# Kernel tuning notes

Measured on AMD Instinct MI355X. Metric: run time of the kernel, lower is better.

The kernel has to match this reference:

```python
import jax, jax.numpy as jnp
import numpy as np

B, T, C = 32, 512, 1024
H, D = 16, 64
BLOCK_SIZE = 512


def setup_inputs() -> dict:
    key = jax.random.key(0)
    ks = jax.random.split(key, 6)
    s_in = 1.0 / np.sqrt(C)
    return {
        "x": jax.random.normal(ks[0], (B, T, C), dtype=jnp.float32),
        "wq": jax.random.normal(ks[1], (H, C, D), dtype=jnp.float32) * s_in,
        "wk": jax.random.normal(ks[2], (H, C, D), dtype=jnp.float32) * s_in,
        "wv": jax.random.normal(ks[3], (H, C, D), dtype=jnp.float32) * s_in,
        "w_proj": jax.random.normal(ks[4], (C, C), dtype=jnp.float32) * s_in,
        "b_proj": jax.random.normal(ks[5], (C,), dtype=jnp.float32) * 0.01,
    }


def reference(x, wq, wk, wv, w_proj, b_proj):
    b, t, c = x.shape
    # per-head projections (bias=False Linears stacked on head axis)
    q = jnp.einsum("btc,hcd->bhtd", x, wq)
    k = jnp.einsum("btc,hcd->bhtd", x, wk)
    v = jnp.einsum("btc,hcd->bhtd", x, wv)
    # NOTE: original scales by 1/sqrt(C) with C = n_embd, not head_size
    scale = 1.0 / (c ** 0.5)
    scores = jnp.einsum("bhtd,bhsd->bhts", q, k) * scale  # [B,H,T,T]
    causal = jnp.tril(jnp.ones((t, t), dtype=bool))
    scores = jnp.where(causal, scores, jnp.finfo(scores.dtype).min)
    attn = jax.nn.softmax(scores, axis=-1)
    out = jnp.einsum("bhts,bhsd->bhtd", attn, v)
    # concat heads in order -> [B,T,H*D]
    out = out.transpose(0, 2, 1, 3).reshape(b, t, -1)
    # output projection (dropout = identity in eval mode)
    return out @ w_proj + b_proj
```

## Files before the change

### kernel.cpp

```cpp
#include <hip/hip_runtime.h>

typedef unsigned int u32;
typedef unsigned short u16;
typedef __bf16 bf16x8 __attribute__((ext_vector_type(8)));
typedef float f32x4 __attribute__((ext_vector_type(4)));
typedef u16 u16x8 __attribute__((ext_vector_type(8)));
typedef u16 u16x4 __attribute__((ext_vector_type(4)));

#define DEVI static __device__ __forceinline__

DEVI u16 f2bf(float f) {
  union { float f; u32 u; } v; v.f = f;
  return (u16)((v.u + 0x7fffu + ((v.u >> 16) & 1u)) >> 16);
}

DEVI u32 cvtpk(float a, float b) {
  u32 r;
  asm("v_cvt_pk_bf16_f32 %0, %1, %2" : "=v"(r) : "v"(a), "v"(b));
  return r;
}

constexpr long QS_ = 16777216;
constexpr long XB_O    = 0;
constexpr long WQKV_O  = 16777216;
constexpr long Q_O     = 19922944;
constexpr long CTX_O   = 70254592;
constexpr long WPROJ_O = 87031808;

__global__ __launch_bounds__(256) void k_prep_all(const float* __restrict__ x,
                                                  const float* __restrict__ wq,
                                                  const float* __restrict__ wk,
                                                  const float* __restrict__ wv,
                                                  const float* __restrict__ wp,
                                                  u16* __restrict__ ws) {
  __shared__ float tile[64][65];
  const int b = blockIdx.x;
  const int tid = threadIdx.x;
  if (b < 1024) {
    const float* src;
    u16* dst;
    long srs;
    if (b < 768) {
      int sel = b >> 8, rest = b & 255, h = rest >> 4, kt = rest & 15;
      const float* W = (sel == 0) ? wq : ((sel == 1) ? wk : wv);
      src = W + (long)(h * 1024 + kt * 64) * 64;
      srs = 64;
      dst = ws + WQKV_O + (long)(sel * 1024 + h * 64) * 1024 + kt * 64;
    } else {
      int b3 = b - 768, ntile = b3 >> 4, kt = b3 & 15;
      src = wp + (long)(kt * 64) * 1024 + ntile * 64;
      srs = 1024;
      dst = ws + WPROJ_O + (long)(ntile * 64) * 1024 + kt * 64;
    }
    #pragma unroll
    for (int i = 0; i < 4; ++i) {
      int idx = i * 256 + tid, r = idx >> 4, c4 = idx & 15;
      float4 v = *(const float4*)(src + (long)r * srs + c4 * 4);
      tile[r][c4 * 4 + 0] = v.x; tile[r][c4 * 4 + 1] = v.y;
      tile[r][c4 * 4 + 2] = v.z; tile[r][c4 * 4 + 3] = v.w;
    }
    __syncthreads();
    #pragma unroll
    for (int i = 0; i < 2; ++i) {
      int idx = i * 256 + tid, dr = idx >> 3, c8 = idx & 7;
      u16x8 o8;
      #pragma unroll
      for (int j = 0; j < 8; ++j) o8[j] = f2bf(tile[c8 * 8 + j][dr]);
      *(u16x8*)(dst + (long)dr * 1024 + c8 * 8) = o8;
    }
  } else {
    long id = (long)(b - 1024) * 256 + tid;
    const float4* p = (const float4*)(x + id * 8);
    float4 a = p[0], c = p[1];
    u16x8 r;
    r[0]=f2bf(a.x); r[1]=f2bf(a.y); r[2]=f2bf(a.z); r[3]=f2bf(a.w);
    r[4]=f2bf(c.x); r[5]=f2bf(c.y); r[6]=f2bf(c.z); r[7]=f2bf(c.w);
    *(u16x8*)(ws + XB_O + id * 8) = r;
  }
}

DEVI void gload16(const u16* g, u16* l) {
  __builtin_amdgcn_global_load_lds((const __attribute__((address_space(1))) u32*)g,
                                   (__attribute__((address_space(3))) u32*)l, 16, 0, 0);
}

template <int NN, int EPI>
__global__ __launch_bounds__(512, 2)
void k_gemm(const u16* __restrict__ A, const u16* __restrict__ Bt,
            u16* __restrict__ oq, float* __restrict__ of, const float* __restrict__ bias) {
  __shared__ u16 lds[2][4][8192];

  const int tid = threadIdx.x;
  const int lane = tid & 63;
  const int w = tid >> 6;
  const int wm = w >> 2, wn = w & 3;
  const int lg = lane >> 4, lr = lane & 15;
  const int bht = 2 + (wn >> 1);
  const int bn0 = (wn & 1) * 4;

  constexpr int NBN = NN / 256;
  const int nwg = gridDim.x;
  const int swz = ((int)blockIdx.x & 7) * (nwg >> 3) + ((int)blockIdx.x >> 3);
  const long m0 = (long)(swz / NBN) * 256, n0 = (long)(swz % NBN) * 256;

  int srcoff[2];
  #pragma unroll
  for (int r2 = 0; r2 < 2; ++r2) {
    int s = r2 * 8 + w;
    int mi = s >> 1, ks = s & 1;
    int rowl = mi * 16 + (lane >> 2);
    int colu = ks * 32 + (((lane & 3) * 8) ^ (((lane >> 5) & 1) * 16));
    srcoff[r2] = rowl * 1024 + colu;
  }
  const int fo = lr * 32 + ((lg * 8) ^ (((lr >> 3) & 1) * 16));

  const u16* At  = A  + m0 * 1024;
  const u16* Bt2 = Bt + n0 * 1024;

  f32x4 acc[8][4] = {};
  bf16x8 aq[2][2][2];
  bf16x8 bfr[4][2];

#define STAGE(buf_, ht_, gbase_)                                               \
  { _Pragma("unroll") for (int r_ = 0; r_ < 2; ++r_)                           \
      gload16((gbase_) + srcoff[r_], &lds[buf_][ht_][r_ * 4096 + w * 512]); }

#define LDS_AQ(set_, buf_, q_)                                                 \
  { _Pragma("unroll") for (int i_ = 0; i_ < 2; ++i_)                           \
    _Pragma("unroll") for (int ks_ = 0; ks_ < 2; ++ks_)                        \
      aq[set_][i_][ks_] = *(const bf16x8*)&lds[buf_][wm][(((q_)*2 + i_) * 2 + ks_) * 512 + fo]; }

#define LDS_BF(buf_, lo_)                                                      \
  { _Pragma("unroll") for (int j_ = 0; j_ < 2; ++j_)                           \
    _Pragma("unroll") for (int ks_ = 0; ks_ < 2; ++ks_)                        \
      bfr[(lo_) + j_][ks_] = *(const bf16x8*)&lds[buf_][bht][((bn0 + (lo_) + j_) * 2 + ks_) * 512 + fo]; }

#define QUAD8(set_, q_, lo_)                                                   \
  { __builtin_amdgcn_s_setprio(1);                                             \
    _Pragma("unroll") for (int ks_ = 0; ks_ < 2; ++ks_)                        \
    _Pragma("unroll") for (int i_ = 0; i_ < 2; ++i_)                           \
    _Pragma("unroll") for (int j_ = 0; j_ < 2; ++j_)                           \
      acc[(q_)*2 + i_][(lo_) + j_] = __builtin_amdgcn_mfma_f32_16x16x32_bf16(  \
          aq[set_][i_][ks_], bfr[(lo_) + j_][ks_], acc[(q_)*2 + i_][(lo_) + j_], 0, 0, 0); \
    __builtin_amdgcn_s_setprio(0); }

#define BARF() { asm volatile("s_barrier" ::: "memory"); }

  STAGE(0, 0, At);
  STAGE(0, 1, At + 131072);
  STAGE(0, 2, Bt2);
  STAGE(0, 3, Bt2 + 131072);
  STAGE(1, 0, At + 64);
  STAGE(1, 1, At + 131072 + 64);
  STAGE(1, 2, Bt2 + 64);
  STAGE(1, 3, Bt2 + 131072 + 64);
  asm volatile("s_waitcnt vmcnt(8)" ::: "memory");
  BARF();
  LDS_AQ(0, 0, 0);
  LDS_BF(0, 0);

  #pragma unroll 1
  for (int t = 0; t < 16; ++t) {
    const int buf = t & 1;
    LDS_BF(buf, 2);
    LDS_AQ(1, buf, 1);
    QUAD8(0, 0, 0);
    BARF();
    QUAD8(0, 0, 2);
    BARF();
    LDS_AQ(0, buf, 2);
    if (t + 2 < 16) { STAGE(buf, 2, Bt2 + (t + 2) * 64); STAGE(buf, 3, Bt2 + 131072 + (t + 2) * 64); }
    QUAD8(1, 1, 0);
    BARF();
    QUAD8(1, 1, 2);
    BARF();
    LDS_AQ(1, buf, 3);
    QUAD8(0, 2, 0);
    BARF();
    QUAD8(0, 2, 2);
    asm volatile("s_waitcnt lgkmcnt(0)" ::: "memory");
    __builtin_amdgcn_sched_barrier(0);
    BARF();
    if (t + 2 < 16) { STAGE(buf, 0, At + (t + 2) * 64); STAGE(buf, 1, At + 131072 + (t + 2) * 64); }
    QUAD8(1, 3, 0);
    BARF();
    if (t < 14)       { asm volatile("s_waitcnt vmcnt(8)" ::: "memory"); }
    else if (t == 14) { asm volatile("s_waitcnt vmcnt(0)" ::: "memory"); }
    BARF();
    if (t + 1 < 16) {
      LDS_AQ(0, buf ^ 1, 0);
      LDS_BF(buf ^ 1, 0);
    }
    QUAD8(1, 3, 2);
    BARF();
  }

  if constexpr (EPI == 0) {
    #pragma unroll
    for (int mi = 0; mi < 8; ++mi) {
      int grow = (int)m0 + wm * 128 + mi * 16 + lg * 4;
      int b = grow >> 9, t0 = grow & 511;
      #pragma unroll
      for (int ni = 0; ni < 4; ++ni) {
        int gcol = (int)n0 + wn * 64 + ni * 16 + lr;
        int sel = gcol >> 10, h = (gcol >> 6) & 15, d = gcol & 63;
        u16* dst = oq + (long)sel * QS_ + (((long)(b * 16 + h) * 512 + t0) * 64 + d);
        #pragma unroll
        for (int r = 0; r < 4; ++r) dst[r * 64] = f2bf(acc[mi][ni][r]);
      }
    }
  } else {
    float bv[4];
    #pragma unroll
    for (int ni = 0; ni < 4; ++ni) bv[ni] = bias[(int)n0 + wn * 64 + ni * 16 + lr];
    #pragma unroll
    for (int mi = 0; mi < 8; ++mi) {
      int grow = (int)m0 + wm * 128 + mi * 16 + lg * 4;
      #pragma unroll
      for (int ni = 0; ni < 4; ++ni) {
        int gcol = (int)n0 + wn * 64 + ni * 16 + lr;
        #pragma unroll
        for (int r = 0; r < 4; ++r)
          of[(long)(grow + r) * NN + gcol] = acc[mi][ni][r] + bv[ni];
      }
    }
  }
#undef STAGE
#undef LDS_AQ
#undef LDS_BF
#undef QUAD8
#undef BARF
}

__global__ __launch_bounds__(256, 3)
void k_attn(const u16* __restrict__ Qp, const u16* __restrict__ Kp,
            const u16* __restrict__ Vp, u16* __restrict__ ctx) {
  __shared__ u16 k_lds[2][64 * 72];
  __shared__ u16 vt_lds[2][64 * 72];

  const int bid = blockIdx.x;
  const int qi = 3 - (bid >> 9);
  const int bh = bid & 511;
  const int tid = threadIdx.x, lane = tid & 63, w = tid >> 6;
  const int lg = lane >> 4, lr = lane & 15;
  const long base = (long)bh * (512 * 64);

  const int q0 = qi * 128 + w * 32;

  bf16x8 qf[2][2];
  #pragma unroll
  for (int mt = 0; mt < 2; ++mt)
    #pragma unroll
    for (int k2 = 0; k2 < 2; ++k2)
      qf[mt][k2] = *(const bf16x8*)(Qp + base + (long)(q0 + mt * 16 + lr) * 64 + k2 * 32 + lg * 8);

  f32x4 o[2][4] = {};
  float ls[2] = {0.f, 0.f};
  u32 pkw[2][4][2];

  const int nch = (qi + 1) * 2;
  int srow[2], scol[2], cslot[2];
  #pragma unroll
  for (int i = 0; i < 2; ++i) {
    int s = i * 256 + tid;
    srow[i] = s >> 3; scol[i] = s & 7;
    int sr = srow[i];
    cslot[i] = ((sr >> 5) << 5) + (((sr >> 2) & 3) << 3) + (((sr >> 4) & 1) << 2) + (sr & 3);
  }

  uint4 kreg[2], vreg[2];
  auto loadch = [&](int c) {
    #pragma unroll
    for (int i = 0; i < 2; ++i) {
      long go = base + (long)(c * 64 + srow[i]) * 64 + scol[i] * 8;
      kreg[i] = *(const uint4*)(Kp + go);
      vreg[i] = *(const uint4*)(Vp + go);
    }
  };
  auto writech = [&](int bsel) {
    #pragma unroll
    for (int i = 0; i < 2; ++i) {
      *(uint4*)&k_lds[bsel][srow[i] * 72 + scol[i] * 8] = kreg[i];
      union { uint4 v; u16 s[8]; } t; t.v = vreg[i];
      #pragma unroll
      for (int j = 0; j < 8; ++j)
        vt_lds[bsel][(scol[i] * 8 + j) * 72 + cslot[i]] = t.s[j];
    }
  };
  auto pv_step = [&](int vsel) {
    bf16x8 vf2[4][2];
    #pragma unroll
    for (int dt = 0; dt < 4; ++dt)
      #pragma unroll
      for (int k2 = 0; k2 < 2; ++k2)
        vf2[dt][k2] = *(const bf16x8*)&vt_lds[vsel][(dt * 16 + lr) * 72 + k2 * 32 + lg * 8];
    __builtin_amdgcn_s_setprio(1);
    #pragma unroll
    for (int k2 = 0; k2 < 2; ++k2)
      #pragma unroll
      for (int mt = 0; mt < 2; ++mt) {
        union { u32 w4[4]; bf16x8 v; } pb;
        pb.w4[0] = pkw[mt][2 * k2][0];
        pb.w4[1] = pkw[mt][2 * k2][1];
        pb.w4[2] = pkw[mt][2 * k2 + 1][0];
        pb.w4[3] = pkw[mt][2 * k2 + 1][1];
        #pragma unroll
        for (int dt = 0; dt < 4; ++dt)
          o[mt][dt] = __builtin_amdgcn_mfma_f32_16x16x32_bf16(vf2[dt][k2], pb.v, o[mt][dt], 0, 0, 0);
      }
    __builtin_amdgcn_s_setprio(0);
  };

  loadch(0);
  writech(0);
  loadch(1);
  __syncthreads();

  const float sc = 0.045084220027780106f;

  #pragma unroll 1
  for (int c = 0; c < nch; ++c) {
    const int bsel = c & 1;
    const bool doQK = (c * 64 <= q0 + 31);
    const bool doPV = (c >= 1) && ((c - 1) * 64 <= q0 + 31);

    f32x4 st[2][4] = {};
    if (doQK) {
      bf16x8 kf2[4][2];
      #pragma unroll
      for (int nt = 0; nt < 4; ++nt)
        #pragma unroll
        for (int k2 = 0; k2 < 2; ++k2)
          kf2[nt][k2] = *(const bf16x8*)&k_lds[bsel][(nt * 16 + lr) * 72 + k2 * 32 + lg * 8];
      __builtin_amdgcn_s_setprio(1);
      #pragma unroll
      for (int k2 = 0; k2 < 2; ++k2)
        #pragma unroll
        for (int mt = 0; mt < 2; ++mt)
          #pragma unroll
          for (int nt = 0; nt < 4; ++nt)
            st[mt][nt] = __builtin_amdgcn_mfma_f32_16x16x32_bf16(kf2[nt][k2], qf[mt][k2], st[mt][nt], 0, 0, 0);
      __builtin_amdgcn_s_setprio(0);
    }

    if (doPV) pv_step(bsel ^ 1);

    if (doQK) {
      const bool full = (c * 64 + 63 <= q0);
      #pragma unroll
      for (int mt = 0; mt < 2; ++mt) {
        const int q = q0 + mt * 16 + lr;
        if (!full) {
          #pragma unroll
          for (int nt = 0; nt < 4; ++nt)
            #pragma unroll
            for (int r = 0; r < 4; ++r) {
              int s_ = c * 64 + nt * 16 + lg * 4 + r;
              st[mt][nt][r] = (s_ <= q) ? st[mt][nt][r] : -1e30f;
            }
        }
        float ps = 0.f;
        float p[4][4];
        #pragma unroll
        for (int nt = 0; nt < 4; ++nt)
          #pragma unroll
          for (int r = 0; r < 4; ++r) {
            float pv = exp2f(st[mt][nt][r] * sc);
            p[nt][r] = pv;
            ps += pv;
          }
        ls[mt] += ps;
        #pragma unroll
        for (int nt = 0; nt < 4; ++nt) {
          pkw[mt][nt][0] = cvtpk(p[nt][0], p[nt][1]);
          pkw[mt][nt][1] = cvtpk(p[nt][2], p[nt][3]);
        }
      }
    }

    __syncthreads();
    if (c + 1 < nch) writech(bsel ^ 1);
    if (c + 2 < nch) loadch(c + 2);
    __syncthreads();
  }

  if ((nch - 1) * 64 <= q0 + 31) pv_step((nch - 1) & 1);

  const int b = bh >> 4, h = bh & 15;
  #pragma unroll
  for (int mt = 0; mt < 2; ++mt) {
    float l = ls[mt];
    l += __shfl_xor(l, 16);
    l += __shfl_xor(l, 32);
    const float inv = 1.0f / l;
    const int t = q0 + mt * 16 + lr;
    #pragma unroll
    for (int dt = 0; dt < 4; ++dt) {
      u16x4 pk4;
      #pragma unroll
      for (int r = 0; r < 4; ++r) pk4[r] = f2bf(o[mt][dt][r] * inv);
      *(u16x4*)(ctx + ((long)(b * 512 + t)) * 1024 + h * 64 + dt * 16 + lg * 4) = pk4;
    }
  }
}

extern "C" void kernel_launch(void* const* d_in, const int* in_sizes, int n_in,
                              void* d_out, int out_size, void* d_ws, size_t ws_size,
                              hipStream_t stream) {
  const float* x  = (const float*)d_in[0];
  const float* wq = (const float*)d_in[1];
  const float* wk = (const float*)d_in[2];
  const float* wv = (const float*)d_in[3];
  const float* wp = (const float*)d_in[4];
  const float* bp = (const float*)d_in[5];
  float* out = (float*)d_out;
  u16* ws = (u16*)d_ws;

  u16* XB    = ws + XB_O;
  u16* WQKV  = ws + WQKV_O;
  u16* Qb    = ws + Q_O;
  u16* CTX   = ws + CTX_O;
  u16* WPROJ = ws + WPROJ_O;

  k_prep_all<<<9216, 256, 0, stream>>>(x, wq, wk, wv, wp, ws);
  k_gemm<3072, 0><<<(16384 / 256) * (3072 / 256), 512, 0, stream>>>(XB, WQKV, Qb, nullptr, nullptr);
  k_attn<<<2048, 256, 0, stream>>>(Qb, Qb + QS_, Qb + 2 * QS_, CTX);
  k_gemm<1024, 1><<<(16384 / 256) * (1024 / 256), 512, 0, stream>>>(CTX, WPROJ, nullptr, out, bp);
}
```

Measured before the change: 221.7 us.

## Load GEMM B fragments from global memory, fold softmax scale into Q, stagger V transpose

The GEMM no longer stages the B (weight) tile through LDS. Each wave loads its B fragments directly from global memory into registers, which halves LDS usage and drops the B staging loads and their waits. The softmax scale (log2e/sqrt(C)) is now folded into the Q epilogue of the QKV GEMM, removing one multiply per score in attention. The V transpose write into LDS rotates its element order per column to reduce bank conflicts. Direct global B loads skip the LDS reuse across waves and may raise global/L2 traffic and latency exposure.

New measurement: 340.4 us. 1.54x slower.

```diff
diff --git a/kernel.cpp b/kernel.cpp
--- a/kernel.cpp
+++ b/kernel.cpp
@@ -26,6 +26,8 @@
 constexpr long Q_O     = 19922944;
 constexpr long CTX_O   = 70254592;
 constexpr long WPROJ_O = 87031808;
+
+#define SCL_Q 0.045084220027780106f
 
 __global__ __launch_bounds__(256) void k_prep_all(const float* __restrict__ x,
                                                   const float* __restrict__ wq,
@@ -88,15 +90,15 @@
 __global__ __launch_bounds__(512, 2)
 void k_gemm(const u16* __restrict__ A, const u16* __restrict__ Bt,
             u16* __restrict__ oq, float* __restrict__ of, const float* __restrict__ bias) {
-  __shared__ u16 lds[2][4][8192];
+  __shared__ u16 lds[2][2][8192];
 
   const int tid = threadIdx.x;
   const int lane = tid & 63;
   const int w = tid >> 6;
   const int wm = w >> 2, wn = w & 3;
   const int lg = lane >> 4, lr = lane & 15;
-  const int bht = 2 + (wn >> 1);
   const int bn0 = (wn & 1) * 4;
+  const int bhtrow = (wn >> 1) * 128;
 
   constexpr int NBN = NN / 256;
   const int nwg = gridDim.x;
@@ -116,6 +118,7 @@
 
   const u16* At  = A  + m0 * 1024;
   const u16* Bt2 = Bt + n0 * 1024;
+  const u16* Bfb = Bt2 + (long)(bhtrow + bn0 * 16 + lr) * 1024 + lg * 8;
 
   f32x4 acc[8][4] = {};
   bf16x8 aq[2][2][2];
@@ -130,10 +133,10 @@
     _Pragma("unroll") for (int ks_ = 0; ks_ < 2; ++ks_)                        \
       aq[set_][i_][ks_] = *(const bf16x8*)&lds[buf_][wm][(((q_)*2 + i_) * 2 + ks_) * 512 + fo]; }
 
-#define LDS_BF(buf_, lo_)                                                      \
+#define GLB_BF(t_, lo_)                                                        \
   { _Pragma("unroll") for (int j_ = 0; j_ < 2; ++j_)                           \
     _Pragma("unroll") for (int ks_ = 0; ks_ < 2; ++ks_)                        \
-      bfr[(lo_) + j_][ks_] = *(const bf16x8*)&lds[buf_][bht][((bn0 + (lo_) + j_) * 2 + ks_) * 512 + fo]; }
+      bfr[(lo_) + j_][ks_] = *(const bf16x8*)(Bfb + ((lo_) + j_) * 16384 + (t_) * 64 + ks_ * 32); }
 
 #define QUAD8(set_, q_, lo_)                                                   \
   { __builtin_amdgcn_s_setprio(1);                                             \
@@ -148,28 +151,23 @@
 
   STAGE(0, 0, At);
   STAGE(0, 1, At + 131072);
-  STAGE(0, 2, Bt2);
-  STAGE(0, 3, Bt2 + 131072);
   STAGE(1, 0, At + 64);
   STAGE(1, 1, At + 131072 + 64);
-  STAGE(1, 2, Bt2 + 64);
-  STAGE(1, 3, Bt2 + 131072 + 64);
-  asm volatile("s_waitcnt vmcnt(8)" ::: "memory");
+  asm volatile("s_waitcnt vmcnt(4)" ::: "memory");
   BARF();
+  GLB_BF(0, 0);
   LDS_AQ(0, 0, 0);
-  LDS_BF(0, 0);
 
   #pragma unroll 1
   for (int t = 0; t < 16; ++t) {
     const int buf = t & 1;
-    LDS_BF(buf, 2);
+    GLB_BF(t, 2);
     LDS_AQ(1, buf, 1);
     QUAD8(0, 0, 0);
     BARF();
     QUAD8(0, 0, 2);
     BARF();
     LDS_AQ(0, buf, 2);
-    if (t + 2 < 16) { STAGE(buf, 2, Bt2 + (t + 2) * 64); STAGE(buf, 3, Bt2 + 131072 + (t + 2) * 64); }
     QUAD8(1, 1, 0);
     BARF();
     QUAD8(1, 1, 2);
@@ -184,12 +182,12 @@
     if (t + 2 < 16) { STAGE(buf, 0, At + (t + 2) * 64); STAGE(buf, 1, At + 131072 + (t + 2) * 64); }
     QUAD8(1, 3, 0);
     BARF();
-    if (t < 14)       { asm volatile("s_waitcnt vmcnt(8)" ::: "memory"); }
+    if (t < 14)       { asm volatile("s_waitcnt vmcnt(4)" ::: "memory"); }
     else if (t == 14) { asm volatile("s_waitcnt vmcnt(0)" ::: "memory"); }
     BARF();
     if (t + 1 < 16) {
+      GLB_BF(t + 1, 0);
       LDS_AQ(0, buf ^ 1, 0);
-      LDS_BF(buf ^ 1, 0);
     }
     QUAD8(1, 3, 2);
     BARF();
@@ -204,9 +202,10 @@
       for (int ni = 0; ni < 4; ++ni) {
         int gcol = (int)n0 + wn * 64 + ni * 16 + lr;
         int sel = gcol >> 10, h = (gcol >> 6) & 15, d = gcol & 63;
+        float scl = (sel == 0) ? SCL_Q : 1.0f;
         u16* dst = oq + (long)sel * QS_ + (((long)(b * 16 + h) * 512 + t0) * 64 + d);
         #pragma unroll
-        for (int r = 0; r < 4; ++r) dst[r * 64] = f2bf(acc[mi][ni][r]);
+        for (int r = 0; r < 4; ++r) dst[r * 64] = f2bf(acc[mi][ni][r] * scl);
       }
     }
   } else {
@@ -227,7 +226,7 @@
   }
 #undef STAGE
 #undef LDS_AQ
-#undef LDS_BF
+#undef GLB_BF
 #undef QUAD8
 #undef BARF
 }
@@ -283,8 +282,10 @@
       *(uint4*)&k_lds[bsel][srow[i] * 72 + scol[i] * 8] = kreg[i];
       union { uint4 v; u16 s[8]; } t; t.v = vreg[i];
       #pragma unroll
-      for (int j = 0; j < 8; ++j)
-        vt_lds[bsel][(scol[i] * 8 + j) * 72 + cslot[i]] = t.s[j];
+      for (int j = 0; j < 8; ++j) {
+        int jj = (j + scol[i]) & 7;
+        vt_lds[bsel][(scol[i] * 8 + jj) * 72 + cslot[i]] = t.s[jj];
+      }
     }
   };
   auto pv_step = [&](int vsel) {
@@ -315,8 +316,6 @@
   writech(0);
   loadch(1);
   __syncthreads();
-
-  const float sc = 0.045084220027780106f;
 
   #pragma unroll 1
   for (int c = 0; c < nch; ++c) {
@@ -365,7 +364,7 @@
         for (int nt = 0; nt < 4; ++nt)
           #pragma unroll
           for (int r = 0; r < 4; ++r) {
-            float pv = exp2f(st[mt][nt][r] * sc);
+            float pv = exp2f(st[mt][nt][r]);
             p[nt][r] = pv;
             ps += pv;
           }
```
